# Kernel tuning notes

Hardware: AMD Instinct MI355X
Metric: run time of the kernel (lower is better)

## Reference

```python
import jax, jax.numpy as jnp
import numpy as np

D = 256; H = 4; HD = 64; WBAND = 64; KLOC = 8; EMAK = 256
SUMDECAY = 0.9; STATEDECAY = 0.9; STEP = 0.5


def _dwconv(x, kern, pad):
    # x: (B,T,D), kern: (D,1,K) cross-correlation taps, causal left pad
    lhs = jnp.transpose(x, (0, 2, 1))
    out = jax.lax.conv_general_dilated(
        lhs, kern, (1,), [(pad, 0)],
        dimension_numbers=('NCH', 'OIH', 'NCH'),
        feature_group_count=x.shape[-1])
    return jnp.transpose(out, (0, 2, 1))


def _ln(x, g, b):
    m = jnp.mean(x, -1, keepdims=True)
    v = jnp.var(x, -1, keepdims=True)
    return (x - m) * jax.lax.rsqrt(v + 1e-5) * g + b


def _lin(x, w, b):
    return jnp.dot(x, w.T) + b


def _forward(parallel_repr, sequential_state, trajectory_summary, conv_w, conv_b,
             qkv_w, qkv_b, mo_w, mo_b, fg_w, fg_b, gkv_w, gkv_b, go_w, go_b,
             comb_w, comb_b, ffn1_w, ffn1_b, ffn2_w, ffn2_b, tr1_w, tr1_b,
             tr2_w, tr2_b, p2s_w, p2s_b, s2p_w, s2p_b,
             ln1_g, ln1_b, ln2_g, ln2_b, ln3_g, ln3_b, ln4_g, ln4_b):
    B, T, _ = parallel_repr.shape
    # Tier 1: local depthwise causal conv (window 8); torch pads both sides then slices [:T] == causal left pad
    local_history = _dwconv(parallel_repr, conv_w, KLOC - 1) + conv_b
    # Tier 2: banded causal attention (keep j in [i-63, i])
    qkv = _lin(parallel_repr, qkv_w, qkv_b).reshape(B, T, 3, H, HD)
    qkv = jnp.transpose(qkv, (2, 0, 3, 1, 4))  # (3,B,H,T,HD)
    q, k, v = qkv[0], qkv[1], qkv[2]
    idx = jnp.arange(T)
    band = (idx[:, None] >= idx[None, :]) & (idx[None, :] > idx[:, None] - WBAND)
    scores = jnp.einsum('bhqd,bhkd->bhqk', q, k) / jnp.sqrt(jnp.float32(HD))
    attn = jax.nn.softmax(jnp.where(band, scores, -1e9), -1)
    med = jnp.einsum('bhqk,bhkd->bhqd', attn, v)
    med = jnp.transpose(med, (0, 2, 1, 3)).reshape(B, T, D)
    med = _lin(med, mo_w, mo_b)
    fg = jax.nn.sigmoid(_lin(jnp.concatenate([parallel_repr, med], -1), fg_w, fg_b))
    medium_out = med * fg
    # Tier 3: causal cumulative (linear-attention style) global concepts
    gkv = _lin(parallel_repr, gkv_w, gkv_b)
    gk, gv = jnp.split(gkv, 2, -1)
    gk = jax.nn.elu(gk) + 1.0
    concepts = jnp.cumsum(gk * gv, 1) / (jnp.cumsum(gk, 1) + 1e-5)
    global_out = _lin(concepts, go_w, go_b)
    combined = _lin(jnp.concatenate([local_history, medium_out, global_out], -1), comb_w, comb_b)
    pr = _ln(parallel_repr + combined, ln1_g, ln1_b)
    # EMA summary via 256-tap causal depthwise conv: w[i] = (1-d)*d^i
    kE = min(T, EMAK)
    taps = (1.0 - SUMDECAY) * SUMDECAY ** jnp.arange(kE, dtype=jnp.float32)
    kern = jnp.broadcast_to(taps[::-1][None, None, :], (D, 1, kE))
    global_summary = _dwconv(pr, kern, kE - 1)
    guidance = _lin(pr, p2s_w, p2s_b)
    cs = jnp.concatenate([pr + 0.3 * guidance, global_summary], -1)
    deltas = jnp.tanh(_lin(jax.nn.gelu(_lin(cs, tr1_w, tr1_b), approximate=False), tr2_w, tr2_b))
    scaled = deltas * STEP
    # state accumulation via conv trick: acc[t] = sum_i d^i * delta[t-i]
    staps = STATEDECAY ** jnp.arange(kE, dtype=jnp.float32)
    skern = jnp.broadcast_to(staps[::-1][None, None, :], (D, 1, kE))
    acc = _dwconv(scaled, skern, kE - 1)
    dpow = STATEDECAY ** jnp.arange(1, T + 1, dtype=jnp.float32)
    pre_ln = sequential_state[:, None, :] * dpow[None, :, None] + acc
    states = _ln(pre_ln, ln3_g, ln3_b)
    seq_g = _lin(states, s2p_w, s2p_b)
    ffn = _lin(jax.nn.gelu(_lin(pr + 0.3 * seq_g, ffn1_w, ffn1_b), approximate=False), ffn2_w, ffn2_b)
    pr_out = _ln(pr + ffn, ln2_g, ln2_b)
    final_state = _ln(states[:, -1, :], ln4_g, ln4_b)
    final_traj = global_summary[:, -1, :]
    return pr_out, final_state, final_traj


def setup_inputs():
    key = jax.random.key(0)
    ks = jax.random.split(key, 20)
    B, T = 4, 2048
    s = 0.02
    def w(i, shape):
        return jax.random.normal(ks[i], shape, jnp.float32) * s
    return {
        'parallel_repr': jax.random.normal(ks[0], (B, T, D), jnp.float32),
        'sequential_state': jax.random.normal(ks[1], (B, D), jnp.float32),
        'trajectory_summary': jax.random.normal(ks[2], (B, D), jnp.float32),
        'conv_w': w(3, (D, 1, KLOC)), 'conv_b': jnp.zeros((D,)),
        'qkv_w': w(4, (3 * D, D)), 'qkv_b': jnp.zeros((3 * D,)),
        'mo_w': w(5, (D, D)), 'mo_b': jnp.zeros((D,)),
        'fg_w': w(6, (D, 2 * D)), 'fg_b': jnp.zeros((D,)),
        'gkv_w': w(7, (2 * D, D)), 'gkv_b': jnp.zeros((2 * D,)),
        'go_w': w(8, (D, D)), 'go_b': jnp.zeros((D,)),
        'comb_w': w(9, (D, 3 * D)), 'comb_b': jnp.zeros((D,)),
        'ffn1_w': w(10, (4 * D, D)), 'ffn1_b': jnp.zeros((4 * D,)),
        'ffn2_w': w(11, (D, 4 * D)), 'ffn2_b': jnp.zeros((D,)),
        'tr1_w': w(12, (2 * D, 2 * D)), 'tr1_b': jnp.zeros((2 * D,)),
        'tr2_w': w(13, (D, 2 * D)), 'tr2_b': jnp.zeros((D,)),
        'p2s_w': w(14, (D, D)), 'p2s_b': jnp.zeros((D,)),
        's2p_w': w(15, (D, D)), 's2p_b': jnp.zeros((D,)),
        'ln1_g': jnp.ones((D,)), 'ln1_b': jnp.zeros((D,)),
        'ln2_g': jnp.ones((D,)), 'ln2_b': jnp.zeros((D,)),
        'ln3_g': jnp.ones((D,)), 'ln3_b': jnp.zeros((D,)),
        'ln4_g': jnp.ones((D,)), 'ln4_b': jnp.zeros((D,)),
    }


def reference(parallel_repr, sequential_state, trajectory_summary, conv_w, conv_b,
              qkv_w, qkv_b, mo_w, mo_b, fg_w, fg_b, gkv_w, gkv_b, go_w, go_b,
              comb_w, comb_b, ffn1_w, ffn1_b, ffn2_w, ffn2_b, tr1_w, tr1_b,
              tr2_w, tr2_b, p2s_w, p2s_b, s2p_w, s2p_b,
              ln1_g, ln1_b, ln2_g, ln2_b, ln3_g, ln3_b, ln4_g, ln4_b):
    return _forward(parallel_repr, sequential_state, trajectory_summary, conv_w, conv_b,
                    qkv_w, qkv_b, mo_w, mo_b, fg_w, fg_b, gkv_w, gkv_b, go_w, go_b,
                    comb_w, comb_b, ffn1_w, ffn1_b, ffn2_w, ffn2_b, tr1_w, tr1_b,
                    tr2_w, tr2_b, p2s_w, p2s_b, s2p_w, s2p_b,
                    ln1_g, ln1_b, ln2_g, ln2_b, ln3_g, ln3_b, ln4_g, ln4_b)
```

## Files before the change

### kernel.cpp

```cpp
#include <hip/hip_runtime.h>
#include <hip/hip_bf16.h>
#include <math.h>

#define D_  256
#define T_  2048
#define B_  4
#define M_  (B_*T_)
#define H_  4
#define HD_ 64

#define NC_ 64
#define LCH (T_/NC_)

enum { OP_NONE=0, OP_SIGMUL=1, OP_ADDAUX=2, OP_AXPBY=3, OP_GELU=4, OP_TANHHALF=5 };

typedef unsigned short u16;
typedef short short8 __attribute__((ext_vector_type(8)));
typedef float f32x4  __attribute__((ext_vector_type(4)));

__device__ __forceinline__ float gelu_f(float x){ return 0.5f*x*(1.0f+erff(x*0.70710678118654752f)); }
__device__ __forceinline__ float sigmoid_f(float x){ return 1.0f/(1.0f+expf(-x)); }

__device__ __forceinline__ unsigned pk2(float a, float b){
    __hip_bfloat162 h = __float22bfloat162_rn(make_float2(a,b));
    union { __hip_bfloat162 h; unsigned u; } c; c.h = h; return c.u;
}
__device__ __forceinline__ float bfu(u16 u){ return __uint_as_float(((unsigned)u)<<16); }
__device__ __forceinline__ u16 bf1(float x){ return (u16)(pk2(x,x)&0xffffu); }

#define OFF_QKV   0u
#define OFF_MO    327680u
#define OFF_FG    393216u
#define OFF_GO    524288u
#define OFF_COMB  589824u
#define OFF_FFN1  786432u
#define OFF_FFN2  1048576u
#define OFF_TR1   1310720u
#define OFF_TR2   1572864u
#define OFF_P2S   1703936u
#define OFF_S2P   1769472u
#define NWELEM    1835008u
#define NXELEM    2097152u
#define CVT_BLKS  3842u
#define CONV_BLKS 2048u

__global__ __launch_bounds__(256) void cvt_conv_k(
    const float* __restrict__ qkv_w, const float* __restrict__ gkv_w,
    const float* __restrict__ qkv_b, const float* __restrict__ gkv_b,
    const float* __restrict__ mo_w,  const float* __restrict__ fg_w,
    const float* __restrict__ go_w,  const float* __restrict__ comb_w,
    const float* __restrict__ ffn1_w,const float* __restrict__ ffn2_w,
    const float* __restrict__ tr1_w, const float* __restrict__ tr2_w,
    const float* __restrict__ p2s_w, const float* __restrict__ s2p_w,
    const float* __restrict__ X,
    const float* __restrict__ conv_w, const float* __restrict__ conv_b,
    u16* __restrict__ Wh, u16* __restrict__ Xh, float* __restrict__ bq,
    u16* __restrict__ LH)
{
    if (blockIdx.x >= CVT_BLKS){
        int idx = (blockIdx.x - CVT_BLKS)*256 + threadIdx.x;
        int d4 = (idx & 63) * 4;
        int bt = idx >> 6;
        int t = bt & (T_-1);
        float a0 = conv_b[d4], a1 = conv_b[d4+1], a2 = conv_b[d4+2], a3 = conv_b[d4+3];
        const float* xp = X + (size_t)bt*D_ + d4;
        #pragma unroll
        for (int j=0;j<8;++j){
            int tt = t - 7 + j;
            if (tt >= 0){
                float4 v = *(const float4*)(xp + (size_t)(j-7)*D_);
                a0 += v.x * conv_w[(d4+0)*8 + j];
                a1 += v.y * conv_w[(d4+1)*8 + j];
                a2 += v.z * conv_w[(d4+2)*8 + j];
                a3 += v.w * conv_w[(d4+3)*8 + j];
            }
        }
        *(uint2*)(LH + (size_t)bt*D_ + d4) = (uint2){ pk2(a0,a1), pk2(a2,a3) };
        return;
    }
    size_t i = ((size_t)blockIdx.x*256 + threadIdx.x)*4;
    if (i < NWELEM){
        const float* s; size_t base;
        if      (i < OFF_MO)  { s=(i<196608)?qkv_w:gkv_w; base=(i<196608)?0:196608; }
        else if (i < OFF_FG)  { s=mo_w;   base=OFF_MO; }
        else if (i < OFF_GO)  { s=fg_w;   base=OFF_FG; }
        else if (i < OFF_COMB){ s=go_w;   base=OFF_GO; }
        else if (i < OFF_FFN1){ s=comb_w; base=OFF_COMB; }
        else if (i < OFF_FFN2){ s=ffn1_w; base=OFF_FFN1; }
        else if (i < OFF_TR1) { s=ffn2_w; base=OFF_FFN2; }
        else if (i < OFF_TR2) { s=tr1_w;  base=OFF_TR1; }
        else if (i < OFF_P2S) { s=tr2_w;  base=OFF_TR2; }
        else if (i < OFF_S2P) { s=p2s_w;  base=OFF_P2S; }
        else                  { s=s2p_w;  base=OFF_S2P; }
        float4 v = *(const float4*)(s + (i-base));
        *(uint2*)(Wh + i) = (uint2){ pk2(v.x,v.y), pk2(v.z,v.w) };
    } else if (i < NWELEM + NXELEM){
        size_t j = i - NWELEM;
        float4 v = *(const float4*)(X + j);
        *(uint2*)(Xh + j) = (uint2){ pk2(v.x,v.y), pk2(v.z,v.w) };
    } else if (i < NWELEM + NXELEM + 1280){
        size_t j = i - (NWELEM + NXELEM);
        #pragma unroll
        for (int k=0;k<4;++k){
            size_t e = j + k;
            bq[e] = (e < 768) ? qkv_b[e] : gkv_b[e-768];
        }
    }
}

__device__ __forceinline__ void gemm_body(
    u16* As, u16* Ws, int bid,
    const u16* __restrict__ A0, const u16* __restrict__ W0, int ldw0, int K0,
    const u16* __restrict__ A1, const u16* __restrict__ W1, int ldw1, int K1,
    const u16* __restrict__ A2, const u16* __restrict__ W2, int ldw2, int K2,
    const float* __restrict__ bias, const void* __restrict__ aux, int aux_bf16,
    void* __restrict__ C, int ldc, int c_bf16, int op, int ncol, int gemmBlocks,
    float* __restrict__ emaCar)
{
    const int q8   = gemmBlocks >> 3;
    const int lid  = (bid & 7)*q8 + (bid >> 3);
    const int brow = lid / ncol;
    const int bcol = lid - brow*ncol;
    const int row0 = brow*128, col0 = bcol*64;

    const int tid  = threadIdx.x;
    const int lane = tid & 63, wid = tid >> 6;
    const int wm = (wid >> 1)*32, wn = (wid & 1)*32;
    const int l15 = lane & 15, l4 = lane >> 4;
    const int rowA = tid >> 2;
    const int scA  = (tid & 3) * 8;
    const int rowW = tid >> 3;
    const int scW  = (tid & 7) * 8;

    f32x4 acc[2][2];
    #pragma unroll
    for (int i=0;i<2;++i)
        #pragma unroll
        for (int j=0;j<2;++j) acc[i][j] = (f32x4){0.f,0.f,0.f,0.f};

    uint4 ra0, ra1, rw0;

    auto loadtile = [&](const u16* A, const u16* W, int ldw, int K, int kb){
        const u16* ga = A + (size_t)(row0+rowA)*K + kb + scA;
        ra0 = *(const uint4*)ga;
        ra1 = *(const uint4*)(ga + 32);
        rw0 = *(const uint4*)(W + (size_t)(col0+rowW)*ldw + kb + scW);
    };
    auto storetile = [&](){
        const int sw = (rowA&7)<<3;
        *(uint4*)&As[(rowA*64 + scA) ^ sw]      = ra0;
        *(uint4*)&As[(rowA*64 + scA + 32) ^ sw] = ra1;
        *(uint4*)&Ws[(rowW*64 + scW) ^ ((rowW&7)<<3)] = rw0;
    };
    auto mfma_tile = [&](){
        #pragma unroll
        for (int ks=0;ks<2;++ks){
            const int koff = ks*32 + l4*8;
            short8 af[2], bf[2];
            #pragma unroll
            for (int f=0;f<2;++f){
                const int ar = wm + f*16 + l15;
                af[f] = *(const short8*)&As[(ar*64 + koff) ^ ((ar&7)<<3)];
                const int brn = wn + f*16 + l15;
                bf[f] = *(const short8*)&Ws[(brn*64 + koff) ^ ((brn&7)<<3)];
            }
            #pragma unroll
            for (int fm=0;fm<2;++fm)
                #pragma unroll
                for (int fn=0;fn<2;++fn)
                    acc[fm][fn] = __builtin_amdgcn_mfma_f32_16x16x32_bf16(
                        af[fm], bf[fn], acc[fm][fn], 0, 0, 0);
        }
    };

    const u16* Ac = A0; const u16* Wc = W0; int ldwc = ldw0, Kc = K0, kb = 0;
    loadtile(Ac, Wc, ldwc, Kc, 0);
    while (true){
        __syncthreads();
        storetile();
        __syncthreads();
        int nkb = kb + 64;
        const u16* nA = Ac; const u16* nW = Wc; int nld = ldwc, nK = Kc;
        bool have_next = true;
        if (nkb >= Kc){
            if (Ac == A0 && A1){ nA = A1; nW = W1; nld = ldw1; nK = K1; nkb = 0; }
            else if (Ac == A1 && A2){ nA = A2; nW = W2; nld = ldw2; nK = K2; nkb = 0; }
            else have_next = false;
        }
        if (have_next) loadtile(nA, nW, nld, nK, nkb);
        mfma_tile();
        if (!have_next) break;
        Ac = nA; Wc = nW; ldwc = nld; Kc = nK; kb = nkb;
    }

    if (c_bf16){
        __syncthreads();
        #pragma unroll
        for (int fn=0;fn<2;++fn){
            const int n = col0 + wn + fn*16 + l15;
            const float bv = bias[n];
            float eacc = 0.f;
            #pragma unroll
            for (int fm=0;fm<2;++fm){
                #pragma unroll
                for (int j=0;j<4;++j){
                    const int mloc = wm + fm*16 + l4*4 + j;
                    const int m = row0 + mloc;
                    float v = acc[fm][fn][j] + bv;
                    if (op==OP_GELU)          v = gelu_f(v);
                    else if (op==OP_TANHHALF) v = 0.5f*tanhf(v);
                    else if (op!=OP_NONE){
                        const size_t ai = (size_t)m*D_ + n;
                        const float a = aux_bf16 ? bfu(((const u16*)aux)[ai])
                                                 : ((const float*)aux)[ai];
                        if (op==OP_SIGMUL)      v = a*sigmoid_f(v);
                        else if (op==OP_ADDAUX) v = v + a;
                        else                    v = a + 0.3f*v;
                    }
                    const u16 hv = bf1(v);
                    const int nloc = wn + fn*16 + l15;
                    As[(mloc*64 + nloc) ^ ((mloc&7)<<3)] = hv;
                    if (emaCar){
                        const int rloc = fm*16 + l4*4 + j;
                        eacc += powf(0.9f, (float)(31 - rloc)) * bfu(hv);
                    }
                }
            }
            if (emaCar){
                eacc += __shfl_xor(eacc, 16);
                eacc += __shfl_xor(eacc, 32);
                if (l4 == 0){
                    const int mw = row0 + wm;
                    const int chunk = (mw >> 5) & (NC_-1);
                    const int bbat  = mw >> 11;
                    emaCar[((size_t)bbat*NC_ + chunk)*D_ + n] = eacc;
                }
            }
        }
        __syncthreads();
        const int rw = tid >> 3;
        const int cw = (tid & 7) * 8;
        #pragma unroll
        for (int pass=0;pass<2;++pass){
            const int mloc = rw + pass*64;
            const int base = (mloc*64 + cw) ^ ((mloc&7)<<3);
            uint4 val = *(const uint4*)&As[base];
            *(uint4*)((u16*)C + (size_t)(row0+mloc)*ldc + col0 + cw) = val;
        }
    } else {
        #pragma unroll
        for (int fn=0;fn<2;++fn){
            const int n = col0 + wn + fn*16 + l15;
            const float bv = bias[n];
            #pragma unroll
            for (int fm=0;fm<2;++fm){
                #pragma unroll
                for (int j=0;j<4;++j){
                    const int m = row0 + wm + fm*16 + l4*4 + j;
                    float v = acc[fm][fn][j] + bv;
                    if (op==OP_GELU)          v = gelu_f(v);
                    else if (op==OP_TANHHALF) v = 0.5f*tanhf(v);
                    else if (op!=OP_NONE){
                        const size_t ai = (size_t)m*D_ + n;
                        const float a = aux_bf16 ? bfu(((const u16*)aux)[ai])
                                                 : ((const float*)aux)[ai];
                        if (op==OP_SIGMUL)      v = a*sigmoid_f(v);
                        else if (op==OP_ADDAUX) v = v + a;
                        else                    v = a + 0.3f*v;
                    }
                    ((float*)C)[(size_t)m*ldc + n] = v;
                }
            }
        }
    }
}

__global__ __launch_bounds__(512) void gemm_k(
    const u16* __restrict__ A0, const u16* __restrict__ W0, int ldw0, int K0,
    const u16* __restrict__ A1, const u16* __restrict__ W1, int ldw1, int K1,
    const u16* __restrict__ A2, const u16* __restrict__ W2, int ldw2, int K2,
    const float* __restrict__ bias, const void* __restrict__ aux, int aux_bf16,
    void* __restrict__ C, int ldc, int c_bf16, int op, int ncol,
    int gemmBlocks, int tailOp,
    const u16* __restrict__ tIn, const float* __restrict__ tC0,
    const float* __restrict__ tC1, u16* __restrict__ tOut, float* __restrict__ tTraj,
    float* __restrict__ emaCar)
{
    if ((int)blockIdx.x >= gemmBlocks){
        if (threadIdx.x < 256){
            const int j = blockIdx.x - gemmBlocks;
            const int c = j & (NC_-1), b = j >> 6;
            const int d = threadIdx.x;
            if (tailOp == 1){
                float sgk = 0.f, sgkv = 0.f;
                for (int cc=0; cc<c; ++cc){
                    sgk  += tC0[((size_t)b*NC_ + cc)*D_ + d];
                    sgkv += tC1[((size_t)b*NC_ + cc)*D_ + d];
                }
                const u16* base = tIn + ((size_t)(b*T_ + c*LCH))*1280;
                u16* out = tOut + ((size_t)(b*T_ + c*LCH))*D_ + d;
                for (int t=0;t<LCH;++t){
                    float gk = bfu(base[(size_t)t*1280 + 768 + d]);
                    gk = gk > 0.f ? gk + 1.f : expf(gk);
                    float gv = bfu(base[(size_t)t*1280 + 1024 + d]);
                    sgk += gk; sgkv += gk*gv;
                    out[(size_t)t*D_] = bf1(sgkv / (sgk + 1e-5f));
                }
            } else {
                const float dL = powf(0.9f, (float)LCH);
                float g = 0.f;
                for (int cc=0; cc<c; ++cc) g = tC0[((size_t)b*NC_ + cc)*D_ + d] + dL*g;
                const u16* xp = tIn + ((size_t)(b*T_ + c*LCH))*D_ + d;
                u16* op2 = tOut + ((size_t)(b*T_ + c*LCH))*D_ + d;
                for (int t=0;t<LCH;++t){
                    g = 0.9f*g + 0.1f*bfu(xp[(size_t)t*D_]);
                    op2[(size_t)t*D_] = bf1(g);
                }
                if (c == NC_-1) tTraj[b*D_ + d] = g;
            }
        }
        return;
    }
    __shared__ u16 As[128*64];
    __shared__ u16 Ws[64*64];
    gemm_body(As, Ws, blockIdx.x,
        A0,W0,ldw0,K0, A1,W1,ldw1,K1, A2,W2,ldw2,K2,
        bias, aux, aux_bf16, C, ldc, c_bf16, op, ncol, gemmBlocks, emaCar);
}

__global__ __launch_bounds__(512) void gemm2_k(
    const u16* __restrict__ CONC, const u16* __restrict__ WGO,
    const float* __restrict__ go_b, u16* __restrict__ GOUT,
    const u16* __restrict__ Xh, const u16* __restrict__ WFG,
    const u16* __restrict__ MED2, const u16* __restrict__ WFG2,
    const float* __restrict__ fg_b, u16* __restrict__ MOUT)
{
    __shared__ u16 As[128*64];
    __shared__ u16 Ws[64*64];
    if ((int)blockIdx.x < 256){
        gemm_body(As, Ws, blockIdx.x,
            CONC, WGO, 256, 256,  nullptr,nullptr,0,0,  nullptr,nullptr,0,0,
            go_b, nullptr, 0, GOUT, 256, 1, OP_NONE, 4, 256, nullptr);
    } else {
        gemm_body(As, Ws, blockIdx.x - 256,
            Xh, WFG, 512, 256,  MED2, WFG2, 512, 256,  nullptr,nullptr,0,0,
            fg_b, MED2, 1, MOUT, 256, 1, OP_SIGMUL, 4, 256, nullptr);
    }
}

__global__ __launch_bounds__(256) void attn_scan_k(const u16* __restrict__ QKVG,
    u16* __restrict__ MED, float* __restrict__ CA, float* __restrict__ CC)
{
    const int tid = threadIdx.x;
    if (blockIdx.x >= 512){
        const int j = blockIdx.x - 512;
        const int c = j & (NC_-1), b = j >> 6;
        const int d = tid;
        const u16* base = QKVG + ((size_t)(b*T_ + c*LCH))*1280;
        float sgk=0.f, sgkv=0.f;
        for (int t=0;t<LCH;++t){
            float gk = bfu(base[(size_t)t*1280 + 768 + d]);
            gk = gk > 0.f ? gk + 1.f : expf(gk);
            float gv = bfu(base[(size_t)t*1280 + 1024 + d]);
            sgk += gk; sgkv += gk*gv;
        }
        CA[((size_t)b*NC_ + c)*D_ + d] = sgk;
        CC[((size_t)b*NC_ + c)*D_ + d] = sgkv;
        return;
    }

    __shared__ u16 Kl[128*64];
    __shared__ u16 Ql[64*64];
    __shared__ u16 Vl[64*128];
    const int b = blockIdx.x >> 7, h = (blockIdx.x >> 5) & 3;
    const int t0 = (blockIdx.x & 31) * 64;
    const int kb0 = t0 - 64;

    {
        const int r0 = tid >> 3, c8 = (tid & 7) * 8;
        #pragma unroll
        for (int rep=0;rep<4;++rep){
            const int r = r0 + rep*32;
            const int kg = kb0 + r;
            uint4 pk = {0,0,0,0}, pv = {0,0,0,0};
            if (kg >= 0){
                const u16* gp = QKVG + ((size_t)(b*T_ + kg))*1280 + h*HD_ + c8;
                pk = *(const uint4*)(gp + 256);
                pv = *(const uint4*)(gp + 512);
            }
            *(uint4*)&Kl[(r*64 + c8) ^ ((r&7)<<3)] = pk;
            const u16* pvu = (const u16*)&pv;
            #pragma unroll
            for (int j=0;j<8;++j){
                const int d = c8 + j;
                Vl[(d*128 + r) ^ ((d&15)<<3)] = pvu[j];
            }
        }
        #pragma unroll
        for (int rep=0;rep<2;++rep){
            const int r = r0 + rep*32;
            uint4 pq = *(const uint4*)(QKVG + ((size_t)(b*T_ + t0 + r))*1280 + h*HD_ + c8);
            *(uint4*)&Ql[(r*64 + c8) ^ ((r&7)<<3)] = pq;
        }
    }
    __syncthreads();

    const int lane = tid & 63, w = tid >> 6;
    const int l15 = lane & 15, l4 = lane >> 4;

    short8 bq[2];
    {
        const int qr = w*16 + l15;
        bq[0] = *(const short8*)&Ql[(qr*64 +      l4*8) ^ ((qr&7)<<3)];
        bq[1] = *(const short8*)&Ql[(qr*64 + 32 + l4*8) ^ ((qr&7)<<3)];
    }

    f32x4 s[8];
    #pragma unroll
    for (int kf=0;kf<8;++kf){
        const int kr = kf*16 + l15;
        short8 a0 = *(const short8*)&Kl[(kr*64 +      l4*8) ^ ((kr&7)<<3)];
        short8 a1 = *(const short8*)&Kl[(kr*64 + 32 + l4*8) ^ ((kr&7)<<3)];
        f32x4 acc = (f32x4){0.f,0.f,0.f,0.f};
        acc = __builtin_amdgcn_mfma_f32_16x16x32_bf16(a0, bq[0], acc, 0,0,0);
        acc = __builtin_amdgcn_mfma_f32_16x16x32_bf16(a1, bq[1], acc, 0,0,0);
        s[kf] = acc;
    }

    const int qg = t0 + w*16 + l15;
    float m = -1e30f;
    #pragma unroll
    for (int kf=0;kf<8;++kf){
        #pragma unroll
        for (int j=0;j<4;++j){
            const int kg = kb0 + kf*16 + l4*4 + j;
            const int diff = qg - kg;
            const float v = (kg >= 0 && diff >= 0 && diff < 64) ? s[kf][j]*0.125f : -1e30f;
            s[kf][j] = v;
            m = fmaxf(m, v);
        }
    }
    m = fmaxf(m, __shfl_xor(m,16));
    m = fmaxf(m, __shfl_xor(m,32));
    float lsum = 0.f;
    unsigned lo[8], hi[8];
    #pragma unroll
    for (int kf=0;kf<8;++kf){
        const float p0 = expf(s[kf][0]-m), p1 = expf(s[kf][1]-m);
        const float p2 = expf(s[kf][2]-m), p3 = expf(s[kf][3]-m);
        lsum += (p0+p1)+(p2+p3);
        lo[kf] = pk2(p0,p1);
        hi[kf] = pk2(p2,p3);
    }
    lsum += __shfl_xor(lsum,16);
    lsum += __shfl_xor(lsum,32);
    const float inv = 1.f/lsum;

    f32x4 o[4];
    #pragma unroll
    for (int df=0;df<4;++df) o[df] = (f32x4){0.f,0.f,0.f,0.f};
    const int baseLane = l15 + ((l4&1)<<5);
    const bool hiHalf = (l4>>1) != 0;
    #pragma unroll
    for (int kb=0;kb<4;++kb){
        const int x0 = __shfl((int)lo[2*kb],   baseLane);
        const int x1 = __shfl((int)hi[2*kb],   baseLane);
        const int x2 = __shfl((int)lo[2*kb],   baseLane+16);
        const int x3 = __shfl((int)hi[2*kb],   baseLane+16);
        const int y0 = __shfl((int)lo[2*kb+1], baseLane);
        const int y1 = __shfl((int)hi[2*kb+1], baseLane);
        const int y2 = __shfl((int)lo[2*kb+1], baseLane+16);
        const int y3 = __shfl((int)hi[2*kb+1], baseLane+16);
        int4 afi;
        afi.x = hiHalf ? y0 : x0;
        afi.y = hiHalf ? y1 : x1;
        afi.z = hiHalf ? y2 : x2;
        afi.w = hiHalf ? y3 : x3;
        union { int4 i; short8 s; } cv; cv.i = afi;
        #pragma unroll
        for (int df=0;df<4;++df){
            const int vr = df*16 + l15;
            short8 bv = *(const short8*)&Vl[(vr*128 + kb*32 + l4*8) ^ ((vr&15)<<3)];
            o[df] = __builtin_amdgcn_mfma_f32_16x16x32_bf16(cv.s, bv, o[df], 0,0,0);
        }
    }

    __syncthreads();
    #pragma unroll
    for (int j=0;j<4;++j){
        const float invj = __shfl(inv, l4*4 + j);
        const int r = w*16 + l4*4 + j;
        #pragma unroll
        for (int df=0;df<4;++df){
            const int dc = df*16 + l15;
            Ql[(r*64 + dc) ^ ((r&7)<<3)] = bf1(o[df][j] * invj);
        }
    }
    __syncthreads();
    {
        const int rw = tid >> 3;
        const int cw = (tid & 7) * 8;
        #pragma unroll
        for (int pass=0;pass<2;++pass){
            const int r = rw + pass*32;
            const int base = (r*64 + cw) ^ ((r&7)<<3);
            uint4 val = *(const uint4*)&Ql[base];
            *(uint4*)(MED + (size_t)(b*T_ + t0 + r)*D_ + h*HD_ + cw) = val;
        }
    }
}

__global__ __launch_bounds__(256) void ln1ema_k(const u16* __restrict__ in,
    const float* __restrict__ g, const float* __restrict__ b,
    u16* __restrict__ out, float* __restrict__ CARRY)
{
    __shared__ float wacc[4][256];
    const int c = blockIdx.x, bb = blockIdx.y;
    const int w = threadIdx.x >> 6, lane = threadIdx.x & 63;
    const int db = lane*4;
    const int row0 = bb*T_ + c*LCH;
    float acc0=0.f, acc1=0.f, acc2=0.f, acc3=0.f;
    #pragma unroll
    for (int it=0; it<8; ++it){
        const int r = it*4 + w;
        uint2 u = *(const uint2*)(in + (size_t)(row0 + r)*D_ + db);
        float x0=bfu((u16)(u.x&0xffff)), x1=bfu((u16)(u.x>>16));
        float x2=bfu((u16)(u.y&0xffff)), x3=bfu((u16)(u.y>>16));
        float s  = x0+x1+x2+x3;
        float s2 = x0*x0+x1*x1+x2*x2+x3*x3;
        #pragma unroll
        for (int o=1;o<64;o<<=1){ s += __shfl_xor(s,o); s2 += __shfl_xor(s2,o); }
        float mean = s*(1.f/256.f);
        float var  = s2*(1.f/256.f) - mean*mean;
        float rs = rsqrtf(var + 1e-5f);
        float y0=(x0-mean)*rs*g[db+0]+b[db+0];
        float y1=(x1-mean)*rs*g[db+1]+b[db+1];
        float y2=(x2-mean)*rs*g[db+2]+b[db+2];
        float y3=(x3-mean)*rs*g[db+3]+b[db+3];
        *(uint2*)(out + (size_t)(row0+r)*D_ + db) = (uint2){ pk2(y0,y1), pk2(y2,y3) };
        const float wt = 0.1f*powf(0.9f, (float)(31-r));
        acc0 += wt*y0; acc1 += wt*y1; acc2 += wt*y2; acc3 += wt*y3;
    }
    wacc[w][db+0]=acc0; wacc[w][db+1]=acc1; wacc[w][db+2]=acc2; wacc[w][db+3]=acc3;
    __syncthreads();
    const int d = threadIdx.x;
    CARRY[((size_t)bb*NC_ + c)*D_ + d] =
        wacc[0][d] + wacc[1][d] + wacc[2][d] + wacc[3][d];
}

__global__ __launch_bounds__(256) void ema_ln3_k(const u16* __restrict__ X,
    const float* __restrict__ CARRY, const float* __restrict__ SEQ,
    const float* __restrict__ g3, const float* __restrict__ b3, u16* __restrict__ states,
    const float* __restrict__ g4, const float* __restrict__ b4, float* __restrict__ fsout)
{
    __shared__ float vals[LCH][256];
    __shared__ float mv[LCH][2];
    __shared__ float st4[256];
    __shared__ float red[8];
    const int d = threadIdx.x, c = blockIdx.x, bb = blockIdx.y;
    const float dL = powf(0.9f, (float)LCH);
    float a = 0.f;
    for (int cc=0; cc<c; ++cc) a = CARRY[((size_t)bb*NC_ + cc)*D_ + d] + dL*a;
    const float ss = SEQ[bb*D_ + d];
    float dp = powf(0.9f, (float)(c*LCH + 1));
    const u16* xp = X + ((size_t)(bb*T_ + c*LCH))*D_ + d;
    for (int t=0;t<LCH;++t){
        a = 0.9f*a + bfu(xp[(size_t)t*D_]);
        vals[t][d] = fmaf(ss, dp, a);
        dp *= 0.9f;
    }
    __syncthreads();
    {
        const int r = threadIdx.x >> 3, seg = threadIdx.x & 7;
        float s=0.f, s2=0.f;
        #pragma unroll
        for (int j=0;j<32;++j){ float v = vals[r][seg*32+j]; s += v; s2 += v*v; }
        s += __shfl_xor(s,1); s2 += __shfl_xor(s2,1);
        s += __shfl_xor(s,2); s2 += __shfl_xor(s2,2);
        s += __shfl_xor(s,4); s2 += __shfl_xor(s2,4);
        if (seg == 0){
            float mean = s*(1.f/256.f);
            float var  = s2*(1.f/256.f) - mean*mean;
            mv[r][0] = mean; mv[r][1] = rsqrtf(var + 1e-5f);
        }
    }
    __syncthreads();
    const float gd = g3[d], bd = b3[d];
    const bool isLast = (c == NC_-1);
    u16* sp = states + ((size_t)(bb*T_ + c*LCH))*D_ + d;
    for (int t=0;t<LCH;++t){
        float st = (vals[t][d] - mv[t][0])*mv[t][1]*gd + bd;
        sp[(size_t)t*D_] = bf1(st);
        if (isLast && t == LCH-1) st4[d] = st;
    }
    if (isLast){
        __syncthreads();
        float v = st4[d];
        float s = v, s2 = v*v;
        #pragma unroll
        for (int o=1;o<64;o<<=1){ s += __shfl_xor(s,o); s2 += __shfl_xor(s2,o); }
        if ((threadIdx.x & 63) == 0){ red[threadIdx.x>>6] = s; red[4+(threadIdx.x>>6)] = s2; }
        __syncthreads();
        float S  = red[0]+red[1]+red[2]+red[3];
        float S2 = red[4]+red[5]+red[6]+red[7];
        float m2 = S*(1.f/256.f);
        float r2 = rsqrtf(S2*(1.f/256.f) - m2*m2 + 1e-5f);
        fsout[bb*D_ + d] = (st4[d]-m2)*r2*g4[d] + b4[d];
    }
}

__global__ __launch_bounds__(256) void ln2h_k(const u16* __restrict__ in,
    const float* __restrict__ g, const float* __restrict__ b, float* __restrict__ out)
{
    int row  = blockIdx.x*4 + (threadIdx.x>>6);
    int lane = threadIdx.x & 63;
    uint2 u = *(const uint2*)(in + (size_t)row*D_ + lane*4);
    float x0=bfu((u16)(u.x&0xffff)), x1=bfu((u16)(u.x>>16));
    float x2=bfu((u16)(u.y&0xffff)), x3=bfu((u16)(u.y>>16));
    float s  = x0+x1+x2+x3;
    float s2 = x0*x0+x1*x1+x2*x2+x3*x3;
    #pragma unroll
    for (int o=1;o<64;o<<=1){ s += __shfl_xor(s,o); s2 += __shfl_xor(s2,o); }
    float mean = s * (1.f/256.f);
    float var  = s2 * (1.f/256.f) - mean*mean;
    float rs = rsqrtf(var + 1e-5f);
    int db = lane*4;
    float4 r;
    r.x=(x0-mean)*rs*g[db+0]+b[db+0];
    r.y=(x1-mean)*rs*g[db+1]+b[db+1];
    r.z=(x2-mean)*rs*g[db+2]+b[db+2];
    r.w=(x3-mean)*rs*g[db+3]+b[db+3];
    *(float4*)(out + (size_t)row*D_ + db) = r;
}

extern "C" void kernel_launch(void* const* d_in, const int* in_sizes, int n_in,
                              void* d_out, int out_size, void* d_ws, size_t ws_size,
                              hipStream_t stream)
{
    const float* X     = (const float*)d_in[0];
    const float* SEQ   = (const float*)d_in[1];
    const float* conv_w= (const float*)d_in[3];
    const float* conv_b= (const float*)d_in[4];
    const float* qkv_w = (const float*)d_in[5];
    const float* qkv_b = (const float*)d_in[6];
    const float* mo_w  = (const float*)d_in[7];
    const float* mo_b  = (const float*)d_in[8];
    const float* fg_w  = (const float*)d_in[9];
    const float* fg_b  = (const float*)d_in[10];
    const float* gkv_w = (const float*)d_in[11];
    const float* gkv_b = (const float*)d_in[12];
    const float* go_w  = (const float*)d_in[13];
    const float* go_b  = (const float*)d_in[14];
    const float* comb_w= (const float*)d_in[15];
    const float* comb_b= (const float*)d_in[16];
    const float* ffn1_w= (const float*)d_in[17];
    const float* ffn1_b= (const float*)d_in[18];
    const float* ffn2_w= (const float*)d_in[19];
    const float* ffn2_b= (const float*)d_in[20];
    const float* tr1_w = (const float*)d_in[21];
    const float* tr1_b = (const float*)d_in[22];
    const float* tr2_w = (const float*)d_in[23];
    const float* tr2_b = (const float*)d_in[24];
    const float* p2s_w = (const float*)d_in[25];
    const float* p2s_b = (const float*)d_in[26];
    const float* s2p_w = (const float*)d_in[27];
    const float* s2p_b = (const float*)d_in[28];
    const float* ln1_g = (const float*)d_in[29];
    const float* ln1_b = (const float*)d_in[30];
    const float* ln2_g = (const float*)d_in[31];
    const float* ln2_b = (const float*)d_in[32];
    const float* ln3_g = (const float*)d_in[33];
    const float* ln3_b = (const float*)d_in[34];
    const float* ln4_g = (const float*)d_in[35];
    const float* ln4_b = (const float*)d_in[36];

    char* p = (char*)d_ws;
    auto alloc = [&](size_t bytes)->char*{ char* r = p; p += (bytes + 255) & ~(size_t)255; return r; };

    u16*   QKVG = (u16*)  alloc((size_t)M_*1280*2);
    u16*   Wh   = (u16*)  alloc((size_t)NWELEM*2);
    float* bq   = (float*)alloc(1280*4);
    u16*   Xh   = (u16*)  alloc((size_t)M_*256*2);
    u16*   MED  = (u16*)  alloc((size_t)M_*256*2);
    u16*   MED2 = (u16*)  alloc((size_t)M_*256*2);
    u16*   LH   = (u16*)  alloc((size_t)M_*256*2);
    u16*   CONC = (u16*)  alloc((size_t)M_*256*2);
    u16*   GOUT = (u16*)  alloc((size_t)M_*256*2);
    u16*   MOUT = (u16*)  alloc((size_t)M_*256*2);
    u16*   PRE1h= (u16*)  alloc((size_t)M_*256*2);
    u16*   PRh  = (u16*)  alloc((size_t)M_*256*2);
    u16*   GSUM = (u16*)  alloc((size_t)M_*256*2);
    u16*   CS1  = (u16*)  alloc((size_t)M_*256*2);
    u16*   H1   = (u16*)  alloc((size_t)M_*512*2);
    u16*   SCALEDh=(u16*) alloc((size_t)M_*256*2);
    u16*   STATESh=(u16*) alloc((size_t)M_*256*2);
    u16*   FFNIN= (u16*)  alloc((size_t)M_*256*2);
    u16*   H2   = (u16*)  alloc((size_t)M_*1024*2);
    u16*   PRE2h= (u16*)  alloc((size_t)M_*256*2);
    float* CAR0 = (float*)alloc((size_t)B_*NC_*D_*4);
    float* CAR1 = (float*)alloc((size_t)B_*NC_*D_*4);

    float* out_pr = (float*)d_out;
    float* out_fs = out_pr + (size_t)M_*256;
    float* out_tj = out_fs + B_*256;

    const dim3 blk256(256), blk512(512);
    const dim3 scan_grid(NC_, B_);
    const int NRg = M_/128;

    cvt_conv_k<<<dim3(CVT_BLKS + CONV_BLKS), blk256, 0, stream>>>(
        qkv_w, gkv_w, qkv_b, gkv_b, mo_w, fg_w, go_w, comb_w,
        ffn1_w, ffn2_w, tr1_w, tr2_w, p2s_w, s2p_w, X, conv_w, conv_b,
        Wh, Xh, bq, LH);
    gemm_k<<<dim3(NRg*20), blk512, 0, stream>>>(
        Xh, Wh+OFF_QKV, 256, 256,  nullptr,nullptr,0,0,  nullptr,nullptr,0,0,
        bq, nullptr, 0, QKVG, 1280, 1, OP_NONE, 20,
        NRg*20, 0, nullptr, nullptr, nullptr, nullptr, nullptr, nullptr);
    attn_scan_k<<<dim3(512 + 256), blk256, 0, stream>>>(QKVG, MED, CAR0, CAR1);
    gemm_k<<<dim3(NRg*4 + 256), blk512, 0, stream>>>(
        MED, Wh+OFF_MO, 256, 256,  nullptr,nullptr,0,0,  nullptr,nullptr,0,0,
        mo_b, nullptr, 0, MED2, 256, 1, OP_NONE, 4,
        NRg*4, 1, QKVG, CAR0, CAR1, CONC, nullptr, nullptr);
    gemm2_k<<<dim3(512), blk512, 0, stream>>>(
        CONC, Wh+OFF_GO, go_b, GOUT,
        Xh, Wh+OFF_FG, MED2, Wh+OFF_FG+256, fg_b, MOUT);
    gemm_k<<<dim3(NRg*4), blk512, 0, stream>>>(
        LH, Wh+OFF_COMB, 768, 256,  MOUT, Wh+OFF_COMB+256, 768, 256,  GOUT, Wh+OFF_COMB+512, 768, 256,
        comb_b, X, 0, PRE1h, 256, 1, OP_ADDAUX, 4,
        NRg*4, 0, nullptr, nullptr, nullptr, nullptr, nullptr, nullptr);
    ln1ema_k<<<scan_grid, blk256, 0, stream>>>(PRE1h, ln1_g, ln1_b, PRh, CAR0);
    gemm_k<<<dim3(NRg*4 + 256), blk512, 0, stream>>>(
        PRh, Wh+OFF_P2S, 256, 256,  nullptr,nullptr,0,0,  nullptr,nullptr,0,0,
        p2s_b, PRh, 1, CS1, 256, 1, OP_AXPBY, 4,
        NRg*4, 2, PRh, CAR0, nullptr, GSUM, out_tj, nullptr);
    gemm_k<<<dim3(NRg*8), blk512, 0, stream>>>(
        CS1, Wh+OFF_TR1, 512, 256,  GSUM, Wh+OFF_TR1+256, 512, 256,  nullptr,nullptr,0,0,
        tr1_b, nullptr, 0, H1, 512, 1, OP_GELU, 8,
        NRg*8, 0, nullptr, nullptr, nullptr, nullptr, nullptr, nullptr);
    gemm_k<<<dim3(NRg*4), blk512, 0, stream>>>(
        H1, Wh+OFF_TR2, 512, 512,  nullptr,nullptr,0,0,  nullptr,nullptr,0,0,
        tr2_b, nullptr, 0, SCALEDh, 256, 1, OP_TANHHALF, 4,
        NRg*4, 0, nullptr, nullptr, nullptr, nullptr, nullptr, CAR0);
    ema_ln3_k<<<scan_grid, blk256, 0, stream>>>(
        SCALEDh, CAR0, SEQ, ln3_g, ln3_b, STATESh, ln4_g, ln4_b, out_fs);
    gemm_k<<<dim3(NRg*4), blk512, 0, stream>>>(
        STATESh, Wh+OFF_S2P, 256, 256,  nullptr,nullptr,0,0,  nullptr,nullptr,0,0,
        s2p_b, PRh, 1, FFNIN, 256, 1, OP_AXPBY, 4,
        NRg*4, 0, nullptr, nullptr, nullptr, nullptr, nullptr, nullptr);
    gemm_k<<<dim3(NRg*16), blk512, 0, stream>>>(
        FFNIN, Wh+OFF_FFN1, 256, 256,  nullptr,nullptr,0,0,  nullptr,nullptr,0,0,
        ffn1_b, nullptr, 0, H2, 1024, 1, OP_GELU, 16,
        NRg*16, 0, nullptr, nullptr, nullptr, nullptr, nullptr, nullptr);
    gemm_k<<<dim3(NRg*4), blk512, 0, stream>>>(
        H2, Wh+OFF_FFN2, 1024, 1024,  nullptr,nullptr,0,0,  nullptr,nullptr,0,0,
        ffn2_b, PRh, 1, PRE2h, 256, 1, OP_ADDAUX, 4,
        NRg*4, 0, nullptr, nullptr, nullptr, nullptr, nullptr, nullptr);
    ln2h_k<<<dim3(M_/4), blk256, 0, stream>>>(PRE2h, ln2_g, ln2_b, out_pr);
}
```

Baseline: 231.7 us.

## Fold p2s and s2p linear layers into downstream tr1 and ffn1 weights

Precomputes combined weights (tr1·(I+0.3·p2s) style and ffn1·0.3·s2p) with small GEMMs launched alongside the QKV projection, plus folded biases. Two full M×256×256 GEMM launches and their intermediate buffers are removed, and the EMA repetition runs in a standalone scan kernel. This trades a small per-call weight-fold cost and extra bf16 rounding of the fused weights for fewer launches and less activation traffic. The folded-bias computation is a serial per-thread loop in the conversion kernel.

```diff
diff --git a/kernel.cpp b/kernel.cpp
--- a/kernel.cpp
+++ b/kernel.cpp
@@ -12,7 +12,7 @@
 #define NC_ 64
 #define LCH (T_/NC_)
 
-enum { OP_NONE=0, OP_SIGMUL=1, OP_ADDAUX=2, OP_AXPBY=3, OP_GELU=4, OP_TANHHALF=5 };
+enum { OP_NONE=0, OP_SIGMUL=1, OP_ADDAUX=2, OP_AXPBY=3, OP_GELU=4, OP_TANHHALF=5, OP_SCALE03=6 };
 
 typedef unsigned short u16;
 typedef short short8 __attribute__((ext_vector_type(8)));
@@ -41,7 +41,9 @@
 #define OFF_S2P   1769472u
 #define NWELEM    1835008u
 #define NXELEM    2097152u
-#define CVT_BLKS  3842u
+#define BQ_END    (NWELEM + NXELEM + 1280u)
+#define BF_END    (BQ_END + 1536u)
+#define CVT_BLKS  3844u
 #define CONV_BLKS 2048u
 
 __global__ __launch_bounds__(256) void cvt_conv_k(
@@ -52,9 +54,12 @@
     const float* __restrict__ ffn1_w,const float* __restrict__ ffn2_w,
     const float* __restrict__ tr1_w, const float* __restrict__ tr2_w,
     const float* __restrict__ p2s_w, const float* __restrict__ s2p_w,
+    const float* __restrict__ tr1_b, const float* __restrict__ p2s_b,
+    const float* __restrict__ ffn1_b,const float* __restrict__ s2p_b,
     const float* __restrict__ X,
     const float* __restrict__ conv_w, const float* __restrict__ conv_b,
     u16* __restrict__ Wh, u16* __restrict__ Xh, float* __restrict__ bq,
+    float* __restrict__ bWA, float* __restrict__ bWF,
     u16* __restrict__ LH)
 {
     if (blockIdx.x >= CVT_BLKS){
@@ -79,7 +84,7 @@
         return;
     }
     size_t i = ((size_t)blockIdx.x*256 + threadIdx.x)*4;
-    if (i < NWELEM){
+    if (i < OFF_P2S){
         const float* s; size_t base;
         if      (i < OFF_MO)  { s=(i<196608)?qkv_w:gkv_w; base=(i<196608)?0:196608; }
         else if (i < OFF_FG)  { s=mo_w;   base=OFF_MO; }
@@ -89,31 +94,58 @@
         else if (i < OFF_FFN2){ s=ffn1_w; base=OFF_FFN1; }
         else if (i < OFF_TR1) { s=ffn2_w; base=OFF_FFN2; }
         else if (i < OFF_TR2) { s=tr1_w;  base=OFF_TR1; }
-        else if (i < OFF_P2S) { s=tr2_w;  base=OFF_TR2; }
-        else if (i < OFF_S2P) { s=p2s_w;  base=OFF_P2S; }
-        else                  { s=s2p_w;  base=OFF_S2P; }
+        else                  { s=tr2_w;  base=OFF_TR2; }
         float4 v = *(const float4*)(s + (i-base));
         *(uint2*)(Wh + i) = (uint2){ pk2(v.x,v.y), pk2(v.z,v.w) };
+    } else if (i < NWELEM){
+        const float* s = (i < OFF_S2P) ? p2s_w : s2p_w;
+        const size_t base = (i < OFF_S2P) ? OFF_P2S : OFF_S2P;
+        const size_t e = i - base;
+        const int n = (int)(e >> 8), k = (int)(e & 255);
+        float4 v = *(const float4*)(s + e);
+        u16* dst = Wh + base;
+        dst[(size_t)(k+0)*256 + n] = bf1(v.x);
+        dst[(size_t)(k+1)*256 + n] = bf1(v.y);
+        dst[(size_t)(k+2)*256 + n] = bf1(v.z);
+        dst[(size_t)(k+3)*256 + n] = bf1(v.w);
     } else if (i < NWELEM + NXELEM){
         size_t j = i - NWELEM;
         float4 v = *(const float4*)(X + j);
         *(uint2*)(Xh + j) = (uint2){ pk2(v.x,v.y), pk2(v.z,v.w) };
-    } else if (i < NWELEM + NXELEM + 1280){
+    } else if (i < BQ_END){
         size_t j = i - (NWELEM + NXELEM);
         #pragma unroll
         for (int k=0;k<4;++k){
             size_t e = j + k;
             bq[e] = (e < 768) ? qkv_b[e] : gkv_b[e-768];
         }
+    } else if (i < BF_END){
+        size_t j = i - BQ_END;
+        #pragma unroll
+        for (int k=0;k<4;++k){
+            const size_t e = j + k;
+            if (e < 512){
+                float acc = tr1_b[e];
+                const float* w = tr1_w + e*512;
+                for (int n=0;n<256;++n) acc += 0.3f*w[n]*p2s_b[n];
+                bWA[e] = acc;
+            } else {
+                const size_t r = e - 512;
+                float acc = ffn1_b[r];
+                const float* w = ffn1_w + r*256;
+                for (int n=0;n<256;++n) acc += 0.3f*w[n]*s2p_b[n];
+                bWF[r] = acc;
+            }
+        }
     }
 }
 
 __device__ __forceinline__ void gemm_body(
     u16* As, u16* Ws, int bid,
-    const u16* __restrict__ A0, const u16* __restrict__ W0, int ldw0, int K0,
-    const u16* __restrict__ A1, const u16* __restrict__ W1, int ldw1, int K1,
-    const u16* __restrict__ A2, const u16* __restrict__ W2, int ldw2, int K2,
-    const float* __restrict__ bias, const void* __restrict__ aux, int aux_bf16,
+    const u16* __restrict__ A0, int lda0, const u16* __restrict__ W0, int ldw0, int K0,
+    const u16* __restrict__ A1, int lda1, const u16* __restrict__ W1, int ldw1, int K1,
+    const u16* __restrict__ A2, int lda2, const u16* __restrict__ W2, int ldw2, int K2,
+    const float* __restrict__ bias, const void* __restrict__ aux, int aux_bf16, int ldaux,
     void* __restrict__ C, int ldc, int c_bf16, int op, int ncol, int gemmBlocks,
     float* __restrict__ emaCar)
 {
@@ -140,8 +172,8 @@
 
     uint4 ra0, ra1, rw0;
 
-    auto loadtile = [&](const u16* A, const u16* W, int ldw, int K, int kb){
-        const u16* ga = A + (size_t)(row0+rowA)*K + kb + scA;
+    auto loadtile = [&](const u16* A, int lda, const u16* W, int ldw, int kb){
+        const u16* ga = A + (size_t)(row0+rowA)*lda + kb + scA;
         ra0 = *(const uint4*)ga;
         ra1 = *(const uint4*)(ga + 32);
         rw0 = *(const uint4*)(W + (size_t)(col0+rowW)*ldw + kb + scW);
@@ -173,24 +205,24 @@
         }
     };
 
-    const u16* Ac = A0; const u16* Wc = W0; int ldwc = ldw0, Kc = K0, kb = 0;
-    loadtile(Ac, Wc, ldwc, Kc, 0);
+    const u16* Ac = A0; const u16* Wc = W0; int ldac = lda0, ldwc = ldw0, Kc = K0, kb = 0;
+    loadtile(Ac, ldac, Wc, ldwc, 0);
     while (true){
         __syncthreads();
         storetile();
         __syncthreads();
         int nkb = kb + 64;
-        const u16* nA = Ac; const u16* nW = Wc; int nld = ldwc, nK = Kc;
+        const u16* nA = Ac; const u16* nW = Wc; int nlda = ldac, nld = ldwc, nK = Kc;
         bool have_next = true;
         if (nkb >= Kc){
-            if (Ac == A0 && A1){ nA = A1; nW = W1; nld = ldw1; nK = K1; nkb = 0; }
-            else if (Ac == A1 && A2){ nA = A2; nW = W2; nld = ldw2; nK = K2; nkb = 0; }
+            if (Ac == A0 && A1){ nA = A1; nW = W1; nlda = lda1; nld = ldw1; nK = K1; nkb = 0; }
+            else if (Ac == A1 && A2){ nA = A2; nW = W2; nlda = lda2; nld = ldw2; nK = K2; nkb = 0; }
             else have_next = false;
         }
-        if (have_next) loadtile(nA, nW, nld, nK, nkb);
+        if (have_next) loadtile(nA, nlda, nW, nld, nkb);
         mfma_tile();
         if (!have_next) break;
-        Ac = nA; Wc = nW; ldwc = nld; Kc = nK; kb = nkb;
+        Ac = nA; Wc = nW; ldac = nlda; ldwc = nld; Kc = nK; kb = nkb;
     }
 
     if (c_bf16){
@@ -198,7 +230,7 @@
         #pragma unroll
         for (int fn=0;fn<2;++fn){
             const int n = col0 + wn + fn*16 + l15;
-            const float bv = bias[n];
+            const float bv = bias ? bias[n] : 0.f;
             float eacc = 0.f;
             #pragma unroll
             for (int fm=0;fm<2;++fm){
@@ -209,8 +241,9 @@
                     float v = acc[fm][fn][j] + bv;
                     if (op==OP_GELU)          v = gelu_f(v);
                     else if (op==OP_TANHHALF) v = 0.5f*tanhf(v);
+                    else if (op==OP_SCALE03)  v = 0.3f*v;
                     else if (op!=OP_NONE){
-                        const size_t ai = (size_t)m*D_ + n;
+                        const size_t ai = (size_t)m*ldaux + n;
                         const float a = aux_bf16 ? bfu(((const u16*)aux)[ai])
                                                  : ((const float*)aux)[ai];
                         if (op==OP_SIGMUL)      v = a*sigmoid_f(v);
@@ -251,7 +284,7 @@
         #pragma unroll
         for (int fn=0;fn<2;++fn){
             const int n = col0 + wn + fn*16 + l15;
-            const float bv = bias[n];
+            const float bv = bias ? bias[n] : 0.f;
             #pragma unroll
             for (int fm=0;fm<2;++fm){
                 #pragma unroll
@@ -260,8 +293,9 @@
                     float v = acc[fm][fn][j] + bv;
                     if (op==OP_GELU)          v = gelu_f(v);
                     else if (op==OP_TANHHALF) v = 0.5f*tanhf(v);
+                    else if (op==OP_SCALE03)  v = 0.3f*v;
                     else if (op!=OP_NONE){
-                        const size_t ai = (size_t)m*D_ + n;
+                        const size_t ai = (size_t)m*ldaux + n;
                         const float a = aux_bf16 ? bfu(((const u16*)aux)[ai])
                                                  : ((const float*)aux)[ai];
                         if (op==OP_SIGMUL)      v = a*sigmoid_f(v);
@@ -324,8 +358,34 @@
     __shared__ u16 As[128*64];
     __shared__ u16 Ws[64*64];
     gemm_body(As, Ws, blockIdx.x,
-        A0,W0,ldw0,K0, A1,W1,ldw1,K1, A2,W2,ldw2,K2,
-        bias, aux, aux_bf16, C, ldc, c_bf16, op, ncol, gemmBlocks, emaCar);
+        A0,K0,W0,ldw0,K0, A1,K1,W1,ldw1,K1, A2,K2,W2,ldw2,K2,
+        bias, aux, aux_bf16, D_, C, ldc, c_bf16, op, ncol, gemmBlocks, emaCar);
+}
+
+__global__ __launch_bounds__(512) void qkvfold_k(
+    const u16* __restrict__ Xh, const u16* __restrict__ Wh,
+    const float* __restrict__ bq, u16* __restrict__ QKVG,
+    u16* __restrict__ WA, u16* __restrict__ WF)
+{
+    __shared__ u16 As[128*64];
+    __shared__ u16 Ws[64*64];
+    const int bid = blockIdx.x;
+    if (bid < 1280){
+        gemm_body(As, Ws, bid,
+            Xh,256, Wh+OFF_QKV,256,256,
+            nullptr,0,nullptr,0,0,  nullptr,0,nullptr,0,0,
+            bq, nullptr, 0, D_, QKVG, 1280, 1, OP_NONE, 20, 1280, nullptr);
+    } else if (bid < 1296){
+        gemm_body(As, Ws, bid-1280,
+            Wh+OFF_TR1,512, Wh+OFF_P2S,256,256,
+            nullptr,0,nullptr,0,0,  nullptr,0,nullptr,0,0,
+            nullptr, Wh+OFF_TR1, 1, 512, WA, 256, 1, OP_AXPBY, 4, 16, nullptr);
+    } else {
+        gemm_body(As, Ws, bid-1296,
+            Wh+OFF_FFN1,256, Wh+OFF_S2P,256,256,
+            nullptr,0,nullptr,0,0,  nullptr,0,nullptr,0,0,
+            nullptr, nullptr, 0, 256, WF, 256, 1, OP_SCALE03, 4, 32, nullptr);
+    }
 }
 
 __global__ __launch_bounds__(512) void gemm2_k(
@@ -339,13 +399,29 @@
     __shared__ u16 Ws[64*64];
     if ((int)blockIdx.x < 256){
         gemm_body(As, Ws, blockIdx.x,
-            CONC, WGO, 256, 256,  nullptr,nullptr,0,0,  nullptr,nullptr,0,0,
-            go_b, nullptr, 0, GOUT, 256, 1, OP_NONE, 4, 256, nullptr);
+            CONC,256, WGO,256,256,  nullptr,0,nullptr,0,0,  nullptr,0,nullptr,0,0,
+            go_b, nullptr, 0, D_, GOUT, 256, 1, OP_NONE, 4, 256, nullptr);
     } else {
         gemm_body(As, Ws, blockIdx.x - 256,
-            Xh, WFG, 512, 256,  MED2, WFG2, 512, 256,  nullptr,nullptr,0,0,
-            fg_b, MED2, 1, MOUT, 256, 1, OP_SIGMUL, 4, 256, nullptr);
-    }
+            Xh,256, WFG,512,256,  MED2,256, WFG2,512,256,  nullptr,0,nullptr,0,0,
+            fg_b, MED2, 1, D_, MOUT, 256, 1, OP_SIGMUL, 4, 256, nullptr);
+    }
+}
+
+__global__ __launch_bounds__(256) void ema_rep_k(const u16* __restrict__ X,
+    const float* __restrict__ CARRY, u16* __restrict__ OUT, float* __restrict__ traj)
+{
+    const int d = threadIdx.x, c = blockIdx.x, b = blockIdx.y;
+    const float dL = powf(0.9f, (float)LCH);
+    float g = 0.f;
+    for (int cc=0; cc<c; ++cc) g = CARRY[((size_t)b*NC_ + cc)*D_ + d] + dL*g;
+    const u16* xp = X + ((size_t)(b*T_ + c*LCH))*D_ + d;
+    u16* op2 = OUT + ((size_t)(b*T_ + c*LCH))*D_ + d;
+    for (int t=0;t<LCH;++t){
+        g = 0.9f*g + 0.1f*bfu(xp[(size_t)t*D_]);
+        op2[(size_t)t*D_] = bf1(g);
+    }
+    if (c == NC_-1) traj[b*D_ + d] = g;
 }
 
 __global__ __launch_bounds__(256) void attn_scan_k(const u16* __restrict__ QKVG,
@@ -680,6 +756,10 @@
     u16*   QKVG = (u16*)  alloc((size_t)M_*1280*2);
     u16*   Wh   = (u16*)  alloc((size_t)NWELEM*2);
     float* bq   = (float*)alloc(1280*4);
+    float* bWA  = (float*)alloc(512*4);
+    float* bWF  = (float*)alloc(1024*4);
+    u16*   WA   = (u16*)  alloc((size_t)512*256*2);
+    u16*   WF   = (u16*)  alloc((size_t)1024*256*2);
     u16*   Xh   = (u16*)  alloc((size_t)M_*256*2);
     u16*   MED  = (u16*)  alloc((size_t)M_*256*2);
     u16*   MED2 = (u16*)  alloc((size_t)M_*256*2);
@@ -690,11 +770,9 @@
     u16*   PRE1h= (u16*)  alloc((size_t)M_*256*2);
     u16*   PRh  = (u16*)  alloc((size_t)M_*256*2);
     u16*   GSUM = (u16*)  alloc((size_t)M_*256*2);
-    u16*   CS1  = (u16*)  alloc((size_t)M_*256*2);
     u16*   H1   = (u16*)  alloc((size_t)M_*512*2);
     u16*   SCALEDh=(u16*) alloc((size_t)M_*256*2);
     u16*   STATESh=(u16*) alloc((size_t)M_*256*2);
-    u16*   FFNIN= (u16*)  alloc((size_t)M_*256*2);
     u16*   H2   = (u16*)  alloc((size_t)M_*1024*2);
     u16*   PRE2h= (u16*)  alloc((size_t)M_*256*2);
     float* CAR0 = (float*)alloc((size_t)B_*NC_*D_*4);
@@ -710,12 +788,11 @@
 
     cvt_conv_k<<<dim3(CVT_BLKS + CONV_BLKS), blk256, 0, stream>>>(
         qkv_w, gkv_w, qkv_b, gkv_b, mo_w, fg_w, go_w, comb_w,
-        ffn1_w, ffn2_w, tr1_w, tr2_w, p2s_w, s2p_w, X, conv_w, conv_b,
-        Wh, Xh, bq, LH);
-    gemm_k<<<dim3(NRg*20), blk512, 0, stream>>>(
-        Xh, Wh+OFF_QKV, 256, 256,  nullptr,nullptr,0,0,  nullptr,nullptr,0,0,
-        bq, nullptr, 0, QKVG, 1280, 1, OP_NONE, 20,
-        NRg*20, 0, nullptr, nullptr, nullptr, nullptr, nullptr, nullptr);
+        ffn1_w, ffn2_w, tr1_w, tr2_w, p2s_w, s2p_w,
+        tr1_b, p2s_b, ffn1_b, s2p_b, X, conv_w, conv_b,
+        Wh, Xh, bq, bWA, bWF, LH);
+    qkvfold_k<<<dim3(1280 + 16 + 32), blk512, 0, stream>>>(
+        Xh, Wh, bq, QKVG, WA, WF);
     attn_scan_k<<<dim3(512 + 256), blk256, 0, stream>>>(QKVG, MED, CAR0, CAR1);
     gemm_k<<<dim3(NRg*4 + 256), blk512, 0, stream>>>(
         MED, Wh+OFF_MO, 256, 256,  nullptr,nullptr,0,0,  nullptr,nullptr,0,0,
@@ -729,13 +806,10 @@
         comb_b, X, 0, PRE1h, 256, 1, OP_ADDAUX, 4,
         NRg*4, 0, nullptr, nullptr, nullptr, nullptr, nullptr, nullptr);
     ln1ema_k<<<scan_grid, blk256, 0, stream>>>(PRE1h, ln1_g, ln1_b, PRh, CAR0);
-    gemm_k<<<dim3(NRg*4 + 256), blk512, 0, stream>>>(
-        PRh, Wh+OFF_P2S, 256, 256,  nullptr,nullptr,0,0,  nullptr,nullptr,0,0,
-        p2s_b, PRh, 1, CS1, 256, 1, OP_AXPBY, 4,
-        NRg*4, 2, PRh, CAR0, nullptr, GSUM, out_tj, nullptr);
+    ema_rep_k<<<scan_grid, blk256, 0, stream>>>(PRh, CAR0, GSUM, out_tj);
     gemm_k<<<dim3(NRg*8), blk512, 0, stream>>>(
-        CS1, Wh+OFF_TR1, 512, 256,  GSUM, Wh+OFF_TR1+256, 512, 256,  nullptr,nullptr,0,0,
-        tr1_b, nullptr, 0, H1, 512, 1, OP_GELU, 8,
+        PRh, WA, 256, 256,  GSUM, Wh+OFF_TR1+256, 512, 256,  nullptr,nullptr,0,0,
+        bWA, nullptr, 0, H1, 512, 1, OP_GELU, 8,
         NRg*8, 0, nullptr, nullptr, nullptr, nullptr, nullptr, nullptr);
     gemm_k<<<dim3(NRg*4), blk512, 0, stream>>>(
         H1, Wh+OFF_TR2, 512, 512,  nullptr,nullptr,0,0,  nullptr,nullptr,0,0,
@@ -743,13 +817,9 @@
         NRg*4, 0, nullptr, nullptr, nullptr, nullptr, nullptr, CAR0);
     ema_ln3_k<<<scan_grid, blk256, 0, stream>>>(
         SCALEDh, CAR0, SEQ, ln3_g, ln3_b, STATESh, ln4_g, ln4_b, out_fs);
-    gemm_k<<<dim3(NRg*4), blk512, 0, stream>>>(
-        STATESh, Wh+OFF_S2P, 256, 256,  nullptr,nullptr,0,0,  nullptr,nullptr,0,0,
-        s2p_b, PRh, 1, FFNIN, 256, 1, OP_AXPBY, 4,
-        NRg*4, 0, nullptr, nullptr, nullptr, nullptr, nullptr, nullptr);
     gemm_k<<<dim3(NRg*16), blk512, 0, stream>>>(
-        FFNIN, Wh+OFF_FFN1, 256, 256,  nullptr,nullptr,0,0,  nullptr,nullptr,0,0,
-        ffn1_b, nullptr, 0, H2, 1024, 1, OP_GELU, 16,
+        PRh, Wh+OFF_FFN1, 256, 256,  STATESh, WF, 256, 256,  nullptr,nullptr,0,0,
+        bWF, nullptr, 0, H2, 1024, 1, OP_GELU, 16,
         NRg*16, 0, nullptr, nullptr, nullptr, nullptr, nullptr, nullptr);
     gemm_k<<<dim3(NRg*4), blk512, 0, stream>>>(
         H2, Wh+OFF_FFN2, 1024, 1024,  nullptr,nullptr,0,0,  nullptr,nullptr,0,0,
```

After: 257.7 us. 1.11x slower.
